# Optimization experiments

Hardware: AMD Instinct MI355X
Metric: run time of the kernel (lower is better)

Reference implementation:

```python
import jax, jax.numpy as jnp
import numpy as np

EXP_CLAMP = 1.0e6
DENOM_EPS = 1e-10
LRELU_ALPHA = 0.01


def setup_inputs() -> dict:
    key = jax.random.key(0)
    k1, k2, k3, k4, k5, k6 = jax.random.split(key, 6)
    B, N, E, F = 4, 16384, 262144, 64
    h = jax.random.normal(k1, (B, N, F), dtype=jnp.float32)
    edge = jax.random.randint(k2, (B, E, 2), 0, N, dtype=jnp.int32)
    edge_num = jax.random.randint(k3, (B,), 1, E, dtype=jnp.int32)
    edge_weight = jax.random.uniform(k4, (B, E), dtype=jnp.float32)
    W = jax.random.normal(k5, (F, F), dtype=jnp.float32) * 0.15  # xavier-ish scale
    a = jax.random.normal(k6, (1, 2 * F), dtype=jnp.float32) * 0.12
    return {"h": h, "edge": edge, "edge_num": edge_num,
            "edge_weight": edge_weight, "W": W, "a": a}


def _seg_sum(src, idx, num_segments):
    # src: [E, ...], idx: [E] -> [num_segments, ...]
    return jax.ops.segment_sum(src, idx, num_segments=num_segments)


def reference(h, edge, edge_num, edge_weight, W, a):
    B, N, Fin = h.shape
    E = edge.shape[1]
    # linear transform: Wh = h @ W^T  -> [B, N, Fout]
    Wh = jnp.einsum('bnf,of->bno', h, W)
    ctr = edge[:, :, 0]  # [B, E]
    nbr = edge[:, :, 1]  # [B, E]
    Wh_c = jnp.take_along_axis(Wh, ctr[:, :, None], axis=1)  # [B, E, Fout]
    Wh_n = jnp.take_along_axis(Wh, nbr[:, :, None], axis=1)  # [B, E, Fout]
    a_input = jnp.concatenate([Wh_c, Wh_n], axis=-1) * edge_weight[:, :, None]
    # attention logits: leakyrelu(a_input @ a^T), squeeze to [B, E]
    att1 = jax.nn.leaky_relu(jnp.einsum('bek,k->be', a_input, a[0]), LRELU_ALPHA)
    # per-batch valid-edge mask (edges beyond edge_num zeroed, as in torch loop)
    mask = (jnp.arange(E, dtype=jnp.int32)[None, :] < edge_num[:, None])
    x_exp = jnp.clip(jnp.exp(att1), 0.0, EXP_CLAMP) * mask.astype(att1.dtype)
    # segment softmax denominator over center nodes
    denom = DENOM_EPS + jax.vmap(_seg_sum, in_axes=(0, 0, None))(x_exp, ctr, N)  # [B, N]
    att = x_exp / jnp.take_along_axis(denom, ctr, axis=1)  # [B, E]
    # weighted neighbor aggregation via scatter-add on center index
    att_Wh = Wh_n * att[:, :, None]  # masked edges already have att == 0
    h_prime = jax.vmap(_seg_sum, in_axes=(0, 0, None))(att_Wh, ctr, N)  # [B, N, Fout]
    return jax.nn.relu(h_prime)
```

## Files before the change

kernel.cpp:

```cpp
#include <hip/hip_runtime.h>

#define BB 4
#define NN 16384
#define EE 262144
#define FF 64
#define ROWS (BB * NN)
#define CAP 64

typedef __bf16 bf16x8 __attribute__((ext_vector_type(8)));
typedef float  f32x4  __attribute__((ext_vector_type(4)));

__device__ __forceinline__ unsigned short f32_to_bf16(float f) {
    unsigned int u = __float_as_uint(f);
    u += 0x7FFFu + ((u >> 16) & 1u);
    return (unsigned short)(u >> 16);
}

__global__ __launch_bounds__(256) void scsn_kernel(
    const float* __restrict__ h, const float* __restrict__ W,
    const float* __restrict__ a,
    float* __restrict__ sc, float* __restrict__ sn, int* __restrict__ cnt)
{
    __shared__ float wc[FF], wn[FF];
    const int t = threadIdx.x;

    if (blockIdx.x < 256) cnt[blockIdx.x * 256 + t] = 0;

    if (t < 128) {
        const int f = t & 63;
        const float* av = a + (t >> 6) * FF;
        float s = 0.0f;
        #pragma unroll 8
        for (int o = 0; o < FF; ++o)
            s = fmaf(av[o], W[o * FF + f], s);
        (t < 64 ? wc : wn)[f] = s;
    }
    __syncthreads();

    const int gl   = t & 15;
    const int rloc = t >> 4;
    const float4 wcv = *(const float4*)&wc[gl * 4];
    const float4 wnv = *(const float4*)&wn[gl * 4];

    for (int base = blockIdx.x * 16; base < ROWS; base += gridDim.x * 16) {
        const int row = base + rloc;
        const float4 hv = ((const float4*)h)[(size_t)row * 16 + gl];
        float s1 = hv.x * wcv.x + hv.y * wcv.y + hv.z * wcv.z + hv.w * wcv.w;
        float s2 = hv.x * wnv.x + hv.y * wnv.y + hv.z * wnv.z + hv.w * wnv.w;
        #pragma unroll
        for (int off = 8; off; off >>= 1) {
            s1 += __shfl_xor(s1, off);
            s2 += __shfl_xor(s2, off);
        }
        if (gl == 0) { sc[row] = s1; sn[row] = s2; }
    }
}

__global__ __launch_bounds__(256) void mfma_bin_kernel(
    const float* __restrict__ h, const float* __restrict__ W,
    const int* __restrict__ edge, const int* __restrict__ edge_num,
    const float* __restrict__ ew,
    const float* __restrict__ sc, const float* __restrict__ sn,
    unsigned short* __restrict__ Wh, int* __restrict__ cnt,
    unsigned int* __restrict__ payload)
{
    const int t = threadIdx.x;
    const int lane = t & 63;
    const int m = lane & 15;
    const int q = lane >> 4;

    bf16x8 bfrag[4][2];
    #pragma unroll
    for (int nt = 0; nt < 4; ++nt) {
        const float* wr = W + (nt * 16 + m) * FF;
        #pragma unroll
        for (int kh = 0; kh < 2; ++kh) {
            const float4 v0 = *(const float4*)(wr + kh * 32 + q * 8);
            const float4 v1 = *(const float4*)(wr + kh * 32 + q * 8 + 4);
            bf16x8 b;
            b[0] = (__bf16)v0.x; b[1] = (__bf16)v0.y;
            b[2] = (__bf16)v0.z; b[3] = (__bf16)v0.w;
            b[4] = (__bf16)v1.x; b[5] = (__bf16)v1.y;
            b[6] = (__bf16)v1.z; b[7] = (__bf16)v1.w;
            bfrag[nt][kh] = b;
        }
    }

    {
        const int waveId = (blockIdx.x * 256 + t) >> 6;
        const int R0 = waveId * 16;
        const float* hr = h + (size_t)(R0 + m) * FF;
        bf16x8 af[2];
        #pragma unroll
        for (int kh = 0; kh < 2; ++kh) {
            const float4 v0 = *(const float4*)(hr + kh * 32 + q * 8);
            const float4 v1 = *(const float4*)(hr + kh * 32 + q * 8 + 4);
            bf16x8 aa;
            aa[0] = (__bf16)v0.x; aa[1] = (__bf16)v0.y;
            aa[2] = (__bf16)v0.z; aa[3] = (__bf16)v0.w;
            aa[4] = (__bf16)v1.x; aa[5] = (__bf16)v1.y;
            aa[6] = (__bf16)v1.z; aa[7] = (__bf16)v1.w;
            af[kh] = aa;
        }
        #pragma unroll
        for (int nt = 0; nt < 4; ++nt) {
            f32x4 acc = {0.f, 0.f, 0.f, 0.f};
            acc = __builtin_amdgcn_mfma_f32_16x16x32_bf16(af[0], bfrag[nt][0], acc, 0, 0, 0);
            acc = __builtin_amdgcn_mfma_f32_16x16x32_bf16(af[1], bfrag[nt][1], acc, 0, 0, 0);
            #pragma unroll
            for (int i = 0; i < 4; ++i)
                Wh[(size_t)(R0 + q * 4 + i) * FF + nt * 16 + m] = f32_to_bf16(acc[i]);
        }
    }

    for (int i2 = blockIdx.x * 256 + t; i2 < (BB * EE) / 2;
         i2 += gridDim.x * 256) {
        const int b  = i2 >> 17;
        const int e0 = (2 * i2) & (EE - 1);
        const int en = edge_num[b];
        if (e0 >= en) continue;
        const int4   e4 = ((const int4*)edge)[i2];
        const float2 w2 = ((const float2*)ew)[i2];
        const int row0 = b * NN + e4.x;
        const int row1 = b * NN + e4.z;
        const bool act1 = (e0 + 1 < en);

        const int pos0 = atomicAdd(&cnt[row0], 1);
        const int pos1 = act1 ? atomicAdd(&cnt[row1], 1) : CAP;

        const float* snB = sn + b * NN;
        float att0 = w2.x * (sc[row0] + snB[e4.y]);
        att0 = att0 > 0.0f ? att0 : 0.01f * att0;
        const float xe0 = fminf(__expf(att0), 1000000.0f);
        unsigned int u0 = (__float_as_uint(xe0) + 0x2000u) & 0xFFFFC000u;
        if (pos0 < CAP)
            payload[(size_t)row0 * CAP + pos0] = u0 | (unsigned int)e4.y;

        if (act1) {
            float att1 = w2.y * (sc[row1] + snB[e4.w]);
            att1 = att1 > 0.0f ? att1 : 0.01f * att1;
            const float xe1 = fminf(__expf(att1), 1000000.0f);
            unsigned int u1 = (__float_as_uint(xe1) + 0x2000u) & 0xFFFFC000u;
            if (pos1 < CAP)
                payload[(size_t)row1 * CAP + pos1] = u1 | (unsigned int)e4.w;
        }
    }
}

__global__ __launch_bounds__(256) void gather_kernel(
    const int* __restrict__ cnt, const unsigned int* __restrict__ payload,
    const uint2* __restrict__ Wh2,
    float* __restrict__ out)
{
    const int bi = blockIdx.x;
    const int xcd = bi & 7;
    const int batch = xcd >> 1;
    const int within = ((bi >> 3) << 1) | (xcd & 1);
    const int rg = batch * 4096 + within;

    const int lane = threadIdx.x & 63;
    const int wave = threadIdx.x >> 6;
    const int row = rg * 4 + wave;
    const int grp = lane >> 4;
    const int gl  = lane & 15;
    int deg = cnt[row];
    if (deg > CAP) deg = CAP;
    const unsigned int* pl = payload + (size_t)row * CAP;
    const uint2* WhB = Wh2 + (size_t)batch * NN * 16;

    float a0 = 0.f, a1 = 0.f, a2 = 0.f, a3 = 0.f, dsum = 0.f;
    const unsigned int p = (lane < deg) ? pl[lane] : 0u;
    for (int jj = 0; jj < deg; jj += 16) {
        const unsigned int pv0 = __shfl(p, jj + grp);
        const unsigned int pv1 = __shfl(p, jj + grp + 4);
        const unsigned int pv2 = __shfl(p, jj + grp + 8);
        const unsigned int pv3 = __shfl(p, jj + grp + 12);
        const uint2 w0 = WhB[(size_t)(pv0 & 0x3FFFu) * 16 + gl];
        const uint2 w1 = WhB[(size_t)(pv1 & 0x3FFFu) * 16 + gl];
        const uint2 w2 = WhB[(size_t)(pv2 & 0x3FFFu) * 16 + gl];
        const uint2 w3 = WhB[(size_t)(pv3 & 0x3FFFu) * 16 + gl];
        const float xe0 = __uint_as_float(pv0 & 0xFFFFC000u);
        const float xe1 = __uint_as_float(pv1 & 0xFFFFC000u);
        const float xe2 = __uint_as_float(pv2 & 0xFFFFC000u);
        const float xe3 = __uint_as_float(pv3 & 0xFFFFC000u);
        a0 = fmaf(xe0, __uint_as_float(w0.x << 16),         a0);
        a1 = fmaf(xe0, __uint_as_float(w0.x & 0xFFFF0000u), a1);
        a2 = fmaf(xe0, __uint_as_float(w0.y << 16),         a2);
        a3 = fmaf(xe0, __uint_as_float(w0.y & 0xFFFF0000u), a3);
        a0 = fmaf(xe1, __uint_as_float(w1.x << 16),         a0);
        a1 = fmaf(xe1, __uint_as_float(w1.x & 0xFFFF0000u), a1);
        a2 = fmaf(xe1, __uint_as_float(w1.y << 16),         a2);
        a3 = fmaf(xe1, __uint_as_float(w1.y & 0xFFFF0000u), a3);
        a0 = fmaf(xe2, __uint_as_float(w2.x << 16),         a0);
        a1 = fmaf(xe2, __uint_as_float(w2.x & 0xFFFF0000u), a1);
        a2 = fmaf(xe2, __uint_as_float(w2.y << 16),         a2);
        a3 = fmaf(xe2, __uint_as_float(w2.y & 0xFFFF0000u), a3);
        a0 = fmaf(xe3, __uint_as_float(w3.x << 16),         a0);
        a1 = fmaf(xe3, __uint_as_float(w3.x & 0xFFFF0000u), a1);
        a2 = fmaf(xe3, __uint_as_float(w3.y << 16),         a2);
        a3 = fmaf(xe3, __uint_as_float(w3.y & 0xFFFF0000u), a3);
        dsum += (xe0 + xe1) + (xe2 + xe3);
    }
    a0 += __shfl_xor(a0, 16); a1 += __shfl_xor(a1, 16);
    a2 += __shfl_xor(a2, 16); a3 += __shfl_xor(a3, 16);
    dsum += __shfl_xor(dsum, 16);
    a0 += __shfl_xor(a0, 32); a1 += __shfl_xor(a1, 32);
    a2 += __shfl_xor(a2, 32); a3 += __shfl_xor(a3, 32);
    dsum += __shfl_xor(dsum, 32);

    if (grp == 0) {
        const float inv = 1.0f / (1e-10f + dsum);
        float4 o;
        o.x = fmaxf(a0 * inv, 0.0f);
        o.y = fmaxf(a1 * inv, 0.0f);
        o.z = fmaxf(a2 * inv, 0.0f);
        o.w = fmaxf(a3 * inv, 0.0f);
        ((float4*)out)[(size_t)row * 16 + gl] = o;
    }
}

extern "C" void kernel_launch(void* const* d_in, const int* in_sizes, int n_in,
                              void* d_out, int out_size, void* d_ws, size_t ws_size,
                              hipStream_t stream)
{
    const float* h        = (const float*)d_in[0];
    const int*   edge     = (const int*)  d_in[1];
    const int*   edge_num = (const int*)  d_in[2];
    const float* ew       = (const float*)d_in[3];
    const float* W        = (const float*)d_in[4];
    const float* a        = (const float*)d_in[5];
    float* out = (float*)d_out;

    unsigned short* Wh = (unsigned short*)d_ws;
    float* sc        = (float*)(Wh + (size_t)BB * NN * FF);
    float* sn        = sc + ROWS;
    int*   cnt       = (int*)(sn + ROWS);
    unsigned int* payload = (unsigned int*)(cnt + ROWS);

    scsn_kernel<<<1024, 256, 0, stream>>>(h, W, a, sc, sn, cnt);

    mfma_bin_kernel<<<1024, 256, 0, stream>>>(h, W, edge, edge_num, ew,
                                              sc, sn, Wh, cnt, payload);

    gather_kernel<<<ROWS / 4, 256, 0, stream>>>(cnt, payload,
                                                (const uint2*)Wh, out);
}
```

Measured before the change: 138.6 us.

## Fold attention scores into MFMA epilogue and defer logit computation to gather

Removes the separate scsn kernel. sc/sn are now computed from the MFMA accumulators by dotting with a and reducing with shuffles. The binning pass stores edge index plus neighbour instead of the precomputed exp weight, and the gather kernel recomputes the attention exp per lane using sc, sn and edge_weight. cnt is zeroed with a memset, and the bin kernel runs with 2048 blocks and one edge pair per thread. This trades a kernel launch and a full pass over h for extra random loads of ew and sn in the gather, and for an Wh-based (bf16-rounded) logit path.

Measured after the change: 148.1 us. 1.07x slower.

```diff
diff --git a/kernel.cpp b/kernel.cpp
--- a/kernel.cpp
+++ b/kernel.cpp
@@ -16,52 +16,12 @@
     return (unsigned short)(u >> 16);
 }
 
-__global__ __launch_bounds__(256) void scsn_kernel(
+__global__ __launch_bounds__(256) void mfma_bin_kernel(
     const float* __restrict__ h, const float* __restrict__ W,
     const float* __restrict__ a,
-    float* __restrict__ sc, float* __restrict__ sn, int* __restrict__ cnt)
-{
-    __shared__ float wc[FF], wn[FF];
-    const int t = threadIdx.x;
-
-    if (blockIdx.x < 256) cnt[blockIdx.x * 256 + t] = 0;
-
-    if (t < 128) {
-        const int f = t & 63;
-        const float* av = a + (t >> 6) * FF;
-        float s = 0.0f;
-        #pragma unroll 8
-        for (int o = 0; o < FF; ++o)
-            s = fmaf(av[o], W[o * FF + f], s);
-        (t < 64 ? wc : wn)[f] = s;
-    }
-    __syncthreads();
-
-    const int gl   = t & 15;
-    const int rloc = t >> 4;
-    const float4 wcv = *(const float4*)&wc[gl * 4];
-    const float4 wnv = *(const float4*)&wn[gl * 4];
-
-    for (int base = blockIdx.x * 16; base < ROWS; base += gridDim.x * 16) {
-        const int row = base + rloc;
-        const float4 hv = ((const float4*)h)[(size_t)row * 16 + gl];
-        float s1 = hv.x * wcv.x + hv.y * wcv.y + hv.z * wcv.z + hv.w * wcv.w;
-        float s2 = hv.x * wnv.x + hv.y * wnv.y + hv.z * wnv.z + hv.w * wnv.w;
-        #pragma unroll
-        for (int off = 8; off; off >>= 1) {
-            s1 += __shfl_xor(s1, off);
-            s2 += __shfl_xor(s2, off);
-        }
-        if (gl == 0) { sc[row] = s1; sn[row] = s2; }
-    }
-}
-
-__global__ __launch_bounds__(256) void mfma_bin_kernel(
-    const float* __restrict__ h, const float* __restrict__ W,
     const int* __restrict__ edge, const int* __restrict__ edge_num,
-    const float* __restrict__ ew,
-    const float* __restrict__ sc, const float* __restrict__ sn,
-    unsigned short* __restrict__ Wh, int* __restrict__ cnt,
+    unsigned short* __restrict__ Wh, float* __restrict__ sc,
+    float* __restrict__ sn, int* __restrict__ cnt,
     unsigned int* __restrict__ payload)
 {
     const int t = threadIdx.x;
@@ -69,25 +29,8 @@
     const int m = lane & 15;
     const int q = lane >> 4;
 
-    bf16x8 bfrag[4][2];
-    #pragma unroll
-    for (int nt = 0; nt < 4; ++nt) {
-        const float* wr = W + (nt * 16 + m) * FF;
-        #pragma unroll
-        for (int kh = 0; kh < 2; ++kh) {
-            const float4 v0 = *(const float4*)(wr + kh * 32 + q * 8);
-            const float4 v1 = *(const float4*)(wr + kh * 32 + q * 8 + 4);
-            bf16x8 b;
-            b[0] = (__bf16)v0.x; b[1] = (__bf16)v0.y;
-            b[2] = (__bf16)v0.z; b[3] = (__bf16)v0.w;
-            b[4] = (__bf16)v1.x; b[5] = (__bf16)v1.y;
-            b[6] = (__bf16)v1.z; b[7] = (__bf16)v1.w;
-            bfrag[nt][kh] = b;
-        }
-    }
-
-    {
-        const int waveId = (blockIdx.x * 256 + t) >> 6;
+    const int waveId = (blockIdx.x * 256 + t) >> 6;
+    if (waveId < ROWS / 16) {
         const int R0 = waveId * 16;
         const float* hr = h + (size_t)(R0 + m) * FF;
         bf16x8 af[2];
@@ -102,54 +45,79 @@
             aa[6] = (__bf16)v1.z; aa[7] = (__bf16)v1.w;
             af[kh] = aa;
         }
+
+        float scv[4] = {0.f, 0.f, 0.f, 0.f};
+        float snv[4] = {0.f, 0.f, 0.f, 0.f};
         #pragma unroll
         for (int nt = 0; nt < 4; ++nt) {
+            const float* wr = W + (nt * 16 + m) * FF;
+            bf16x8 bf[2];
+            #pragma unroll
+            for (int kh = 0; kh < 2; ++kh) {
+                const float4 v0 = *(const float4*)(wr + kh * 32 + q * 8);
+                const float4 v1 = *(const float4*)(wr + kh * 32 + q * 8 + 4);
+                bf16x8 b;
+                b[0] = (__bf16)v0.x; b[1] = (__bf16)v0.y;
+                b[2] = (__bf16)v0.z; b[3] = (__bf16)v0.w;
+                b[4] = (__bf16)v1.x; b[5] = (__bf16)v1.y;
+                b[6] = (__bf16)v1.z; b[7] = (__bf16)v1.w;
+                bf[kh] = b;
+            }
             f32x4 acc = {0.f, 0.f, 0.f, 0.f};
-            acc = __builtin_amdgcn_mfma_f32_16x16x32_bf16(af[0], bfrag[nt][0], acc, 0, 0, 0);
-            acc = __builtin_amdgcn_mfma_f32_16x16x32_bf16(af[1], bfrag[nt][1], acc, 0, 0, 0);
-            #pragma unroll
-            for (int i = 0; i < 4; ++i)
+            acc = __builtin_amdgcn_mfma_f32_16x16x32_bf16(af[0], bf[0], acc, 0, 0, 0);
+            acc = __builtin_amdgcn_mfma_f32_16x16x32_bf16(af[1], bf[1], acc, 0, 0, 0);
+
+            const float acm = a[nt * 16 + m];
+            const float anm = a[FF + nt * 16 + m];
+            #pragma unroll
+            for (int i = 0; i < 4; ++i) {
                 Wh[(size_t)(R0 + q * 4 + i) * FF + nt * 16 + m] = f32_to_bf16(acc[i]);
-        }
-    }
-
-    for (int i2 = blockIdx.x * 256 + t; i2 < (BB * EE) / 2;
-         i2 += gridDim.x * 256) {
-        const int b  = i2 >> 17;
-        const int e0 = (2 * i2) & (EE - 1);
-        const int en = edge_num[b];
-        if (e0 >= en) continue;
-        const int4   e4 = ((const int4*)edge)[i2];
-        const float2 w2 = ((const float2*)ew)[i2];
+                scv[i] = fmaf(acc[i], acm, scv[i]);
+                snv[i] = fmaf(acc[i], anm, snv[i]);
+            }
+        }
+        #pragma unroll
+        for (int i = 0; i < 4; ++i) {
+            #pragma unroll
+            for (int off = 1; off < 16; off <<= 1) {
+                scv[i] += __shfl_xor(scv[i], off);
+                snv[i] += __shfl_xor(snv[i], off);
+            }
+        }
+        if (m == 0) {
+            #pragma unroll
+            for (int i = 0; i < 4; ++i) {
+                sc[R0 + q * 4 + i] = scv[i];
+                sn[R0 + q * 4 + i] = snv[i];
+            }
+        }
+    }
+
+    const int i2 = blockIdx.x * 256 + t;
+    const int b  = i2 >> 17;
+    const int e0 = (2 * i2) & (EE - 1);
+    const int en = edge_num[b];
+    if (e0 < en) {
+        const int4 e4 = ((const int4*)edge)[i2];
         const int row0 = b * NN + e4.x;
-        const int row1 = b * NN + e4.z;
+        const int pos0 = atomicAdd(&cnt[row0], 1);
         const bool act1 = (e0 + 1 < en);
-
-        const int pos0 = atomicAdd(&cnt[row0], 1);
-        const int pos1 = act1 ? atomicAdd(&cnt[row1], 1) : CAP;
-
-        const float* snB = sn + b * NN;
-        float att0 = w2.x * (sc[row0] + snB[e4.y]);
-        att0 = att0 > 0.0f ? att0 : 0.01f * att0;
-        const float xe0 = fminf(__expf(att0), 1000000.0f);
-        unsigned int u0 = (__float_as_uint(xe0) + 0x2000u) & 0xFFFFC000u;
+        int pos1 = CAP, row1 = 0;
+        if (act1) { row1 = b * NN + e4.z; pos1 = atomicAdd(&cnt[row1], 1); }
         if (pos0 < CAP)
-            payload[(size_t)row0 * CAP + pos0] = u0 | (unsigned int)e4.y;
-
-        if (act1) {
-            float att1 = w2.y * (sc[row1] + snB[e4.w]);
-            att1 = att1 > 0.0f ? att1 : 0.01f * att1;
-            const float xe1 = fminf(__expf(att1), 1000000.0f);
-            unsigned int u1 = (__float_as_uint(xe1) + 0x2000u) & 0xFFFFC000u;
-            if (pos1 < CAP)
-                payload[(size_t)row1 * CAP + pos1] = u1 | (unsigned int)e4.w;
-        }
+            payload[(size_t)row0 * CAP + pos0] =
+                ((unsigned int)e0 << 14) | (unsigned int)e4.y;
+        if (act1 && pos1 < CAP)
+            payload[(size_t)row1 * CAP + pos1] =
+                ((unsigned int)(e0 + 1) << 14) | (unsigned int)e4.w;
     }
 }
 
 __global__ __launch_bounds__(256) void gather_kernel(
     const int* __restrict__ cnt, const unsigned int* __restrict__ payload,
     const uint2* __restrict__ Wh2,
+    const float* __restrict__ sc, const float* __restrict__ sn,
+    const float* __restrict__ ew,
     float* __restrict__ out)
 {
     const int bi = blockIdx.x;
@@ -168,8 +136,21 @@
     const unsigned int* pl = payload + (size_t)row * CAP;
     const uint2* WhB = Wh2 + (size_t)batch * NN * 16;
 
+    const unsigned int praw = (lane < deg) ? pl[lane] : 0u;
+    float xe;
+    {
+        const int eidx = (int)(praw >> 14);
+        const int nbr  = (int)(praw & 0x3FFFu);
+        const float we = ew[(size_t)batch * EE + eidx];
+        float att = we * (sc[row] + sn[batch * NN + nbr]);
+        att = att > 0.0f ? att : 0.01f * att;
+        xe = fminf(__expf(att), 1000000.0f);
+        if (lane >= deg) xe = 0.0f;
+    }
+    const unsigned int p = ((__float_as_uint(xe) + 0x2000u) & 0xFFFFC000u)
+                         | (praw & 0x3FFFu);
+
     float a0 = 0.f, a1 = 0.f, a2 = 0.f, a3 = 0.f, dsum = 0.f;
-    const unsigned int p = (lane < deg) ? pl[lane] : 0u;
     for (int jj = 0; jj < deg; jj += 16) {
         const unsigned int pv0 = __shfl(p, jj + grp);
         const unsigned int pv1 = __shfl(p, jj + grp + 4);
@@ -237,11 +218,11 @@
     int*   cnt       = (int*)(sn + ROWS);
     unsigned int* payload = (unsigned int*)(cnt + ROWS);
 
-    scsn_kernel<<<1024, 256, 0, stream>>>(h, W, a, sc, sn, cnt);
-
-    mfma_bin_kernel<<<1024, 256, 0, stream>>>(h, W, edge, edge_num, ew,
-                                              sc, sn, Wh, cnt, payload);
-
-    gather_kernel<<<ROWS / 4, 256, 0, stream>>>(cnt, payload,
-                                                (const uint2*)Wh, out);
-}
+    hipMemsetAsync(cnt, 0, sizeof(int) * ROWS, stream);
+
+    mfma_bin_kernel<<<2048, 256, 0, stream>>>(h, W, a, edge, edge_num,
+                                              Wh, sc, sn, cnt, payload);
+
+    gather_kernel<<<ROWS / 4, 256, 0, stream>>>(cnt, payload, (const uint2*)Wh,
+                                                sc, sn, ew, out);
+}
```

## Split per-row edge bins into eight per-XCD copies to localize atomics

Applied to the files above, without the earlier changes.

The single counter and payload bin arrays are replaced by eight copies, one per XCD group chosen from the block index, each with a capacity of 32 slots. Binning atomics then hit counters that are mostly touched by one XCD, which is meant to cut cross-XCD contention and coherence traffic. The gather kernel reads the eight counts, builds a prefix sum with shuffles, and fetches each lane's payload from the right sub-bin. This costs eight times the counter zeroing and memory, adds extra gather-side work, and truncates edges differently when one sub-bin exceeds 32 entries.

Result: slower. 143.4 us (+3.5%).

```diff
diff --git a/kernel.cpp b/kernel.cpp
--- a/kernel.cpp
+++ b/kernel.cpp
@@ -5,7 +5,7 @@
 #define EE 262144
 #define FF 64
 #define ROWS (BB * NN)
-#define CAP 64
+#define CAPX 32
 
 typedef __bf16 bf16x8 __attribute__((ext_vector_type(8)));
 typedef float  f32x4  __attribute__((ext_vector_type(4)));
@@ -19,12 +19,13 @@
 __global__ __launch_bounds__(256) void scsn_kernel(
     const float* __restrict__ h, const float* __restrict__ W,
     const float* __restrict__ a,
-    float* __restrict__ sc, float* __restrict__ sn, int* __restrict__ cnt)
+    float* __restrict__ sc, float* __restrict__ sn, int* __restrict__ cntx)
 {
     __shared__ float wc[FF], wn[FF];
     const int t = threadIdx.x;
 
-    if (blockIdx.x < 256) cnt[blockIdx.x * 256 + t] = 0;
+    for (int i = blockIdx.x * 256 + t; i < 8 * ROWS; i += 1024 * 256)
+        cntx[i] = 0;
 
     if (t < 128) {
         const int f = t & 63;
@@ -61,8 +62,8 @@
     const int* __restrict__ edge, const int* __restrict__ edge_num,
     const float* __restrict__ ew,
     const float* __restrict__ sc, const float* __restrict__ sn,
-    unsigned short* __restrict__ Wh, int* __restrict__ cnt,
-    unsigned int* __restrict__ payload)
+    unsigned short* __restrict__ Wh, int* __restrict__ cntx,
+    unsigned int* __restrict__ payx)
 {
     const int t = threadIdx.x;
     const int lane = t & 63;
@@ -112,6 +113,10 @@
                 Wh[(size_t)(R0 + q * 4 + i) * FF + nt * 16 + m] = f32_to_bf16(acc[i]);
         }
     }
+
+    const int xg = blockIdx.x & 7;
+    int* cnt = cntx + xg * ROWS;
+    unsigned int* pay = payx + (size_t)xg * ROWS * CAPX;
 
     for (int i2 = blockIdx.x * 256 + t; i2 < (BB * EE) / 2;
          i2 += gridDim.x * 256) {
@@ -126,29 +131,29 @@
         const bool act1 = (e0 + 1 < en);
 
         const int pos0 = atomicAdd(&cnt[row0], 1);
-        const int pos1 = act1 ? atomicAdd(&cnt[row1], 1) : CAP;
+        const int pos1 = act1 ? atomicAdd(&cnt[row1], 1) : CAPX;
 
         const float* snB = sn + b * NN;
         float att0 = w2.x * (sc[row0] + snB[e4.y]);
         att0 = att0 > 0.0f ? att0 : 0.01f * att0;
         const float xe0 = fminf(__expf(att0), 1000000.0f);
         unsigned int u0 = (__float_as_uint(xe0) + 0x2000u) & 0xFFFFC000u;
-        if (pos0 < CAP)
-            payload[(size_t)row0 * CAP + pos0] = u0 | (unsigned int)e4.y;
+        if (pos0 < CAPX)
+            pay[(size_t)row0 * CAPX + pos0] = u0 | (unsigned int)e4.y;
 
         if (act1) {
             float att1 = w2.y * (sc[row1] + snB[e4.w]);
             att1 = att1 > 0.0f ? att1 : 0.01f * att1;
             const float xe1 = fminf(__expf(att1), 1000000.0f);
             unsigned int u1 = (__float_as_uint(xe1) + 0x2000u) & 0xFFFFC000u;
-            if (pos1 < CAP)
-                payload[(size_t)row1 * CAP + pos1] = u1 | (unsigned int)e4.w;
+            if (pos1 < CAPX)
+                pay[(size_t)row1 * CAPX + pos1] = u1 | (unsigned int)e4.w;
         }
     }
 }
 
 __global__ __launch_bounds__(256) void gather_kernel(
-    const int* __restrict__ cnt, const unsigned int* __restrict__ payload,
+    const int* __restrict__ cntx, const unsigned int* __restrict__ payx,
     const uint2* __restrict__ Wh2,
     float* __restrict__ out)
 {
@@ -163,13 +168,40 @@
     const int row = rg * 4 + wave;
     const int grp = lane >> 4;
     const int gl  = lane & 15;
-    int deg = cnt[row];
-    if (deg > CAP) deg = CAP;
-    const unsigned int* pl = payload + (size_t)row * CAP;
     const uint2* WhB = Wh2 + (size_t)batch * NN * 16;
 
+    int myc = 0;
+    if (lane < 8) myc = cntx[lane * ROWS + row];
+    int pref1, pref2, pref3, pref4, pref5, pref6, pref7, pref8;
+    {
+        const int d0 = min(__shfl(myc, 0), CAPX);
+        const int d1 = min(__shfl(myc, 1), CAPX);
+        const int d2 = min(__shfl(myc, 2), CAPX);
+        const int d3 = min(__shfl(myc, 3), CAPX);
+        const int d4 = min(__shfl(myc, 4), CAPX);
+        const int d5 = min(__shfl(myc, 5), CAPX);
+        const int d6 = min(__shfl(myc, 6), CAPX);
+        const int d7 = min(__shfl(myc, 7), CAPX);
+        pref1 = d0;         pref2 = pref1 + d1; pref3 = pref2 + d2;
+        pref4 = pref3 + d3; pref5 = pref4 + d4; pref6 = pref5 + d5;
+        pref7 = pref6 + d6; pref8 = pref7 + d7;
+    }
+    int deg = min(pref8, 64);
+
+    unsigned int p = 0u;
+    if (lane < deg) {
+        int seg = 0, base = 0;
+        if (lane >= pref1) { seg = 1; base = pref1; }
+        if (lane >= pref2) { seg = 2; base = pref2; }
+        if (lane >= pref3) { seg = 3; base = pref3; }
+        if (lane >= pref4) { seg = 4; base = pref4; }
+        if (lane >= pref5) { seg = 5; base = pref5; }
+        if (lane >= pref6) { seg = 6; base = pref6; }
+        if (lane >= pref7) { seg = 7; base = pref7; }
+        p = payx[(size_t)seg * ROWS * CAPX + (size_t)row * CAPX + (lane - base)];
+    }
+
     float a0 = 0.f, a1 = 0.f, a2 = 0.f, a3 = 0.f, dsum = 0.f;
-    const unsigned int p = (lane < deg) ? pl[lane] : 0u;
     for (int jj = 0; jj < deg; jj += 16) {
         const unsigned int pv0 = __shfl(p, jj + grp);
         const unsigned int pv1 = __shfl(p, jj + grp + 4);
@@ -234,14 +266,14 @@
     unsigned short* Wh = (unsigned short*)d_ws;
     float* sc        = (float*)(Wh + (size_t)BB * NN * FF);
     float* sn        = sc + ROWS;
-    int*   cnt       = (int*)(sn + ROWS);
-    unsigned int* payload = (unsigned int*)(cnt + ROWS);
-
-    scsn_kernel<<<1024, 256, 0, stream>>>(h, W, a, sc, sn, cnt);
+    int*   cntx      = (int*)(sn + ROWS);
+    unsigned int* payx = (unsigned int*)(cntx + 8 * ROWS);
+
+    scsn_kernel<<<1024, 256, 0, stream>>>(h, W, a, sc, sn, cntx);
 
     mfma_bin_kernel<<<1024, 256, 0, stream>>>(h, W, edge, edge_num, ew,
-                                              sc, sn, Wh, cnt, payload);
-
-    gather_kernel<<<ROWS / 4, 256, 0, stream>>>(cnt, payload,
+                                              sc, sn, Wh, cntx, payx);
+
+    gather_kernel<<<ROWS / 4, 256, 0, stream>>>(cntx, payx,
                                                 (const uint2*)Wh, out);
 }
```

## Replace capped per-row atomic binning with two-level counting sort into CSR

Applied to the files above, without the earlier changes.

Replaces the fixed-capacity per-row payload slots, filled with global atomics, by a two-level counting sort. Edges are first histogrammed into 256 coarse buckets per chunk, a scan produces offsets, edges are scattered into the buckets, and a per-bucket LDS sort orders them by row to build CSR start offsets. The gather then walks variable-length row ranges and no longer truncates at 64 neighbours. This removes contended global atomics and the scattered payload writes. In exchange it adds two kernel launches, a serial single-block scan, and extra memory traffic for the bucket arrays.

New measurement: 161.1 us. +16.3%, slower.

```diff
diff --git a/kernel.cpp b/kernel.cpp
--- a/kernel.cpp
+++ b/kernel.cpp
@@ -5,7 +5,9 @@
 #define EE 262144
 #define FF 64
 #define ROWS (BB * NN)
-#define CAP 64
+#define CHUNKS 512
+#define CHUNK_E 2048
+#define BCAP 5120
 
 typedef __bf16 bf16x8 __attribute__((ext_vector_type(8)));
 typedef float  f32x4  __attribute__((ext_vector_type(4)));
@@ -16,15 +18,15 @@
     return (unsigned short)(u >> 16);
 }
 
-__global__ __launch_bounds__(256) void scsn_kernel(
+__global__ __launch_bounds__(256) void scsn_hist_kernel(
     const float* __restrict__ h, const float* __restrict__ W,
     const float* __restrict__ a,
-    float* __restrict__ sc, float* __restrict__ sn, int* __restrict__ cnt)
+    const int* __restrict__ edge, const int* __restrict__ edge_num,
+    float* __restrict__ sc, float* __restrict__ sn, int* __restrict__ histArr)
 {
     __shared__ float wc[FF], wn[FF];
+    __shared__ int lhist[256];
     const int t = threadIdx.x;
-
-    if (blockIdx.x < 256) cnt[blockIdx.x * 256 + t] = 0;
 
     if (t < 128) {
         const int f = t & 63;
@@ -41,7 +43,6 @@
     const int rloc = t >> 4;
     const float4 wcv = *(const float4*)&wc[gl * 4];
     const float4 wnv = *(const float4*)&wn[gl * 4];
-
     for (int base = blockIdx.x * 16; base < ROWS; base += gridDim.x * 16) {
         const int row = base + rloc;
         const float4 hv = ((const float4*)h)[(size_t)row * 16 + gl];
@@ -54,39 +55,53 @@
         }
         if (gl == 0) { sc[row] = s1; sn[row] = s2; }
     }
-}
-
-__global__ __launch_bounds__(256) void mfma_bin_kernel(
+
+    if (blockIdx.x < CHUNKS) {
+        lhist[t] = 0;
+        __syncthreads();
+        const int b  = blockIdx.x >> 7;
+        const int en = edge_num[b];
+        const int geBase = blockIdx.x * CHUNK_E;
+        #pragma unroll
+        for (int k = 0; k < 8; ++k) {
+            const int ge = geBase + t + k * 256;
+            if ((ge & (EE - 1)) < en) {
+                const int ctr = edge[2 * (size_t)ge];
+                atomicAdd(&lhist[(b << 6) | (ctr >> 8)], 1);
+            }
+        }
+        __syncthreads();
+        histArr[blockIdx.x * 256 + t] = lhist[t];
+    }
+}
+
+__global__ __launch_bounds__(256) void mfma_scan_kernel(
     const float* __restrict__ h, const float* __restrict__ W,
-    const int* __restrict__ edge, const int* __restrict__ edge_num,
-    const float* __restrict__ ew,
-    const float* __restrict__ sc, const float* __restrict__ sn,
-    unsigned short* __restrict__ Wh, int* __restrict__ cnt,
-    unsigned int* __restrict__ payload)
+    unsigned short* __restrict__ Wh,
+    int* __restrict__ histArr, int* __restrict__ bucketBase,
+    int* __restrict__ startArr)
 {
     const int t = threadIdx.x;
-    const int lane = t & 63;
-    const int m = lane & 15;
-    const int q = lane >> 4;
-
-    bf16x8 bfrag[4][2];
-    #pragma unroll
-    for (int nt = 0; nt < 4; ++nt) {
-        const float* wr = W + (nt * 16 + m) * FF;
-        #pragma unroll
-        for (int kh = 0; kh < 2; ++kh) {
-            const float4 v0 = *(const float4*)(wr + kh * 32 + q * 8);
-            const float4 v1 = *(const float4*)(wr + kh * 32 + q * 8 + 4);
-            bf16x8 b;
-            b[0] = (__bf16)v0.x; b[1] = (__bf16)v0.y;
-            b[2] = (__bf16)v0.z; b[3] = (__bf16)v0.w;
-            b[4] = (__bf16)v1.x; b[5] = (__bf16)v1.y;
-            b[6] = (__bf16)v1.z; b[7] = (__bf16)v1.w;
-            bfrag[nt][kh] = b;
-        }
-    }
-
-    {
+    if (blockIdx.x < 1024) {
+        const int lane = t & 63;
+        const int m = lane & 15;
+        const int q = lane >> 4;
+        bf16x8 bfrag[4][2];
+        #pragma unroll
+        for (int nt = 0; nt < 4; ++nt) {
+            const float* wr = W + (nt * 16 + m) * FF;
+            #pragma unroll
+            for (int kh = 0; kh < 2; ++kh) {
+                const float4 v0 = *(const float4*)(wr + kh * 32 + q * 8);
+                const float4 v1 = *(const float4*)(wr + kh * 32 + q * 8 + 4);
+                bf16x8 b;
+                b[0] = (__bf16)v0.x; b[1] = (__bf16)v0.y;
+                b[2] = (__bf16)v0.z; b[3] = (__bf16)v0.w;
+                b[4] = (__bf16)v1.x; b[5] = (__bf16)v1.y;
+                b[6] = (__bf16)v1.z; b[7] = (__bf16)v1.w;
+                bfrag[nt][kh] = b;
+            }
+        }
         const int waveId = (blockIdx.x * 256 + t) >> 6;
         const int R0 = waveId * 16;
         const float* hr = h + (size_t)(R0 + m) * FF;
@@ -111,46 +126,110 @@
             for (int i = 0; i < 4; ++i)
                 Wh[(size_t)(R0 + q * 4 + i) * FF + nt * 16 + m] = f32_to_bf16(acc[i]);
         }
-    }
-
-    for (int i2 = blockIdx.x * 256 + t; i2 < (BB * EE) / 2;
-         i2 += gridDim.x * 256) {
-        const int b  = i2 >> 17;
-        const int e0 = (2 * i2) & (EE - 1);
-        const int en = edge_num[b];
-        if (e0 >= en) continue;
-        const int4   e4 = ((const int4*)edge)[i2];
-        const float2 w2 = ((const float2*)ew)[i2];
-        const int row0 = b * NN + e4.x;
-        const int row1 = b * NN + e4.z;
-        const bool act1 = (e0 + 1 < en);
-
-        const int pos0 = atomicAdd(&cnt[row0], 1);
-        const int pos1 = act1 ? atomicAdd(&cnt[row1], 1) : CAP;
-
-        const float* snB = sn + b * NN;
-        float att0 = w2.x * (sc[row0] + snB[e4.y]);
-        att0 = att0 > 0.0f ? att0 : 0.01f * att0;
-        const float xe0 = fminf(__expf(att0), 1000000.0f);
-        unsigned int u0 = (__float_as_uint(xe0) + 0x2000u) & 0xFFFFC000u;
-        if (pos0 < CAP)
-            payload[(size_t)row0 * CAP + pos0] = u0 | (unsigned int)e4.y;
-
-        if (act1) {
-            float att1 = w2.y * (sc[row1] + snB[e4.w]);
-            att1 = att1 > 0.0f ? att1 : 0.01f * att1;
-            const float xe1 = fminf(__expf(att1), 1000000.0f);
-            unsigned int u1 = (__float_as_uint(xe1) + 0x2000u) & 0xFFFFC000u;
-            if (pos1 < CAP)
-                payload[(size_t)row1 * CAP + pos1] = u1 | (unsigned int)e4.w;
-        }
-    }
+    } else {
+        __shared__ int sarr[256];
+        int run = 0;
+        for (int blk = 0; blk < CHUNKS; ++blk) {
+            const int idx = blk * 256 + t;
+            const int v = histArr[idx];
+            histArr[idx] = run;
+            run += v;
+        }
+        sarr[t] = run;
+        __syncthreads();
+        int excl = 0;
+        for (int i = 0; i < 256; ++i) {
+            const int v = sarr[i];
+            if (i < t) excl += v;
+        }
+        bucketBase[t] = excl;
+        if (t == 255) {
+            bucketBase[256] = excl + run;
+            startArr[ROWS] = excl + run;
+        }
+    }
+}
+
+__global__ __launch_bounds__(256) void scatter_kernel(
+    const int* __restrict__ edge, const int* __restrict__ edge_num,
+    const float* __restrict__ ew,
+    const float* __restrict__ sc, const float* __restrict__ sn,
+    const int* __restrict__ histArr, const int* __restrict__ bucketBase,
+    unsigned int* __restrict__ bucketArr, unsigned char* __restrict__ rowlowArr)
+{
+    __shared__ int lbase[256];
+    const int t = threadIdx.x;
+    lbase[t] = histArr[blockIdx.x * 256 + t] + bucketBase[t];
+    __syncthreads();
+
+    const int b  = blockIdx.x >> 7;
+    const int en = edge_num[b];
+    const float* snB = sn + b * NN;
+    const int geBase = blockIdx.x * CHUNK_E;
+    #pragma unroll
+    for (int k = 0; k < 8; ++k) {
+        const int ge = geBase + t + k * 256;
+        if ((ge & (EE - 1)) >= en) continue;
+        const int2 e2 = ((const int2*)edge)[ge];
+        const int row = b * NN + e2.x;
+        float att = ew[ge] * (sc[row] + snB[e2.y]);
+        att = att > 0.0f ? att : 0.01f * att;
+        const float xe = fminf(__expf(att), 1000000.0f);
+        const unsigned int u =
+            ((__float_as_uint(xe) + 0x2000u) & 0xFFFFC000u) | (unsigned int)e2.y;
+        const int bkt = (b << 6) | (e2.x >> 8);
+        const int dst = atomicAdd(&lbase[bkt], 1);
+        bucketArr[dst] = u;
+        rowlowArr[dst] = (unsigned char)(e2.x & 255);
+    }
+}
+
+__global__ __launch_bounds__(256) void bsort_kernel(
+    const unsigned int* __restrict__ bucketArr,
+    const unsigned char* __restrict__ rowlowArr,
+    const int* __restrict__ bucketBase,
+    unsigned int* __restrict__ payloadG, int* __restrict__ startArr)
+{
+    __shared__ unsigned int lpay[BCAP];
+    __shared__ unsigned int lsort[BCAP];
+    __shared__ unsigned char llow[BCAP];
+    __shared__ int lhist[256];
+    __shared__ int rankb[256];
+    const int t = threadIdx.x;
+    const int bkt = blockIdx.x;
+    const int base = bucketBase[bkt];
+    int S = bucketBase[bkt + 1] - base;
+    if (S > BCAP) S = BCAP;
+
+    lhist[t] = 0;
+    __syncthreads();
+    for (int i = t; i < S; i += 256) {
+        lpay[i] = bucketArr[base + i];
+        const unsigned char lo = rowlowArr[base + i];
+        llow[i] = lo;
+        atomicAdd(&lhist[lo], 1);
+    }
+    __syncthreads();
+    int excl = 0;
+    for (int i = 0; i < 256; ++i) {
+        const int v = lhist[i];
+        if (i < t) excl += v;
+    }
+    rankb[t] = excl;
+    startArr[bkt * 256 + t] = base + excl;
+    __syncthreads();
+    for (int i = t; i < S; i += 256) {
+        const int d = atomicAdd(&rankb[llow[i]], 1);
+        lsort[d] = lpay[i];
+    }
+    __syncthreads();
+    for (int i = t; i < S; i += 256)
+        payloadG[base + i] = lsort[i];
 }
 
 __global__ __launch_bounds__(256) void gather_kernel(
-    const int* __restrict__ cnt, const unsigned int* __restrict__ payload,
-    const uint2* __restrict__ Wh2,
-    float* __restrict__ out)
+    const int* __restrict__ startArr, const unsigned int* __restrict__ payloadG,
+    const uint2* __restrict__ Wh2, float* __restrict__ out)
 {
     const int bi = blockIdx.x;
     const int xcd = bi & 7;
@@ -163,43 +242,46 @@
     const int row = rg * 4 + wave;
     const int grp = lane >> 4;
     const int gl  = lane & 15;
-    int deg = cnt[row];
-    if (deg > CAP) deg = CAP;
-    const unsigned int* pl = payload + (size_t)row * CAP;
+    const int s = startArr[row];
+    const int e = startArr[row + 1];
     const uint2* WhB = Wh2 + (size_t)batch * NN * 16;
 
     float a0 = 0.f, a1 = 0.f, a2 = 0.f, a3 = 0.f, dsum = 0.f;
-    const unsigned int p = (lane < deg) ? pl[lane] : 0u;
-    for (int jj = 0; jj < deg; jj += 16) {
-        const unsigned int pv0 = __shfl(p, jj + grp);
-        const unsigned int pv1 = __shfl(p, jj + grp + 4);
-        const unsigned int pv2 = __shfl(p, jj + grp + 8);
-        const unsigned int pv3 = __shfl(p, jj + grp + 12);
-        const uint2 w0 = WhB[(size_t)(pv0 & 0x3FFFu) * 16 + gl];
-        const uint2 w1 = WhB[(size_t)(pv1 & 0x3FFFu) * 16 + gl];
-        const uint2 w2 = WhB[(size_t)(pv2 & 0x3FFFu) * 16 + gl];
-        const uint2 w3 = WhB[(size_t)(pv3 & 0x3FFFu) * 16 + gl];
-        const float xe0 = __uint_as_float(pv0 & 0xFFFFC000u);
-        const float xe1 = __uint_as_float(pv1 & 0xFFFFC000u);
-        const float xe2 = __uint_as_float(pv2 & 0xFFFFC000u);
-        const float xe3 = __uint_as_float(pv3 & 0xFFFFC000u);
-        a0 = fmaf(xe0, __uint_as_float(w0.x << 16),         a0);
-        a1 = fmaf(xe0, __uint_as_float(w0.x & 0xFFFF0000u), a1);
-        a2 = fmaf(xe0, __uint_as_float(w0.y << 16),         a2);
-        a3 = fmaf(xe0, __uint_as_float(w0.y & 0xFFFF0000u), a3);
-        a0 = fmaf(xe1, __uint_as_float(w1.x << 16),         a0);
-        a1 = fmaf(xe1, __uint_as_float(w1.x & 0xFFFF0000u), a1);
-        a2 = fmaf(xe1, __uint_as_float(w1.y << 16),         a2);
-        a3 = fmaf(xe1, __uint_as_float(w1.y & 0xFFFF0000u), a3);
-        a0 = fmaf(xe2, __uint_as_float(w2.x << 16),         a0);
-        a1 = fmaf(xe2, __uint_as_float(w2.x & 0xFFFF0000u), a1);
-        a2 = fmaf(xe2, __uint_as_float(w2.y << 16),         a2);
-        a3 = fmaf(xe2, __uint_as_float(w2.y & 0xFFFF0000u), a3);
-        a0 = fmaf(xe3, __uint_as_float(w3.x << 16),         a0);
-        a1 = fmaf(xe3, __uint_as_float(w3.x & 0xFFFF0000u), a1);
-        a2 = fmaf(xe3, __uint_as_float(w3.y << 16),         a2);
-        a3 = fmaf(xe3, __uint_as_float(w3.y & 0xFFFF0000u), a3);
-        dsum += (xe0 + xe1) + (xe2 + xe3);
+    for (int chunk = s; chunk < e; chunk += 64) {
+        const int j = chunk + lane;
+        const unsigned int p = (j < e) ? payloadG[j] : 0u;
+        const int cend = min(64, e - chunk);
+        for (int jj = 0; jj < cend; jj += 16) {
+            const unsigned int pv0 = __shfl(p, jj + grp);
+            const unsigned int pv1 = __shfl(p, jj + grp + 4);
+            const unsigned int pv2 = __shfl(p, jj + grp + 8);
+            const unsigned int pv3 = __shfl(p, jj + grp + 12);
+            const uint2 w0 = WhB[(size_t)(pv0 & 0x3FFFu) * 16 + gl];
+            const uint2 w1 = WhB[(size_t)(pv1 & 0x3FFFu) * 16 + gl];
+            const uint2 w2 = WhB[(size_t)(pv2 & 0x3FFFu) * 16 + gl];
+            const uint2 w3 = WhB[(size_t)(pv3 & 0x3FFFu) * 16 + gl];
+            const float xe0 = __uint_as_float(pv0 & 0xFFFFC000u);
+            const float xe1 = __uint_as_float(pv1 & 0xFFFFC000u);
+            const float xe2 = __uint_as_float(pv2 & 0xFFFFC000u);
+            const float xe3 = __uint_as_float(pv3 & 0xFFFFC000u);
+            a0 = fmaf(xe0, __uint_as_float(w0.x << 16),         a0);
+            a1 = fmaf(xe0, __uint_as_float(w0.x & 0xFFFF0000u), a1);
+            a2 = fmaf(xe0, __uint_as_float(w0.y << 16),         a2);
+            a3 = fmaf(xe0, __uint_as_float(w0.y & 0xFFFF0000u), a3);
+            a0 = fmaf(xe1, __uint_as_float(w1.x << 16),         a0);
+            a1 = fmaf(xe1, __uint_as_float(w1.x & 0xFFFF0000u), a1);
+            a2 = fmaf(xe1, __uint_as_float(w1.y << 16),         a2);
+            a3 = fmaf(xe1, __uint_as_float(w1.y & 0xFFFF0000u), a3);
+            a0 = fmaf(xe2, __uint_as_float(w2.x << 16),         a0);
+            a1 = fmaf(xe2, __uint_as_float(w2.x & 0xFFFF0000u), a1);
+            a2 = fmaf(xe2, __uint_as_float(w2.y << 16),         a2);
+            a3 = fmaf(xe2, __uint_as_float(w2.y & 0xFFFF0000u), a3);
+            a0 = fmaf(xe3, __uint_as_float(w3.x << 16),         a0);
+            a1 = fmaf(xe3, __uint_as_float(w3.x & 0xFFFF0000u), a1);
+            a2 = fmaf(xe3, __uint_as_float(w3.y << 16),         a2);
+            a3 = fmaf(xe3, __uint_as_float(w3.y & 0xFFFF0000u), a3);
+            dsum += (xe0 + xe1) + (xe2 + xe3);
+        }
     }
     a0 += __shfl_xor(a0, 16); a1 += __shfl_xor(a1, 16);
     a2 += __shfl_xor(a2, 16); a3 += __shfl_xor(a3, 16);
@@ -234,14 +316,26 @@
     unsigned short* Wh = (unsigned short*)d_ws;
     float* sc        = (float*)(Wh + (size_t)BB * NN * FF);
     float* sn        = sc + ROWS;
-    int*   cnt       = (int*)(sn + ROWS);
-    unsigned int* payload = (unsigned int*)(cnt + ROWS);
-
-    scsn_kernel<<<1024, 256, 0, stream>>>(h, W, a, sc, sn, cnt);
-
-    mfma_bin_kernel<<<1024, 256, 0, stream>>>(h, W, edge, edge_num, ew,
-                                              sc, sn, Wh, cnt, payload);
-
-    gather_kernel<<<ROWS / 4, 256, 0, stream>>>(cnt, payload,
+    int*   histArr   = (int*)(sn + ROWS);
+    int*   bucketBase= histArr + CHUNKS * 256;
+    int*   startArr  = bucketBase + 260;
+    unsigned int* bucketArr = (unsigned int*)(startArr + ROWS + 4);
+    unsigned char* rowlowArr = (unsigned char*)(bucketArr + BB * EE);
+    unsigned int* payloadG = (unsigned int*)(rowlowArr + BB * EE);
+
+    scsn_hist_kernel<<<1024, 256, 0, stream>>>(h, W, a, edge, edge_num,
+                                               sc, sn, histArr);
+
+    mfma_scan_kernel<<<1025, 256, 0, stream>>>(h, W, Wh, histArr, bucketBase,
+                                               startArr);
+
+    scatter_kernel<<<CHUNKS, 256, 0, stream>>>(edge, edge_num, ew, sc, sn,
+                                               histArr, bucketBase,
+                                               bucketArr, rowlowArr);
+
+    bsort_kernel<<<256, 256, 0, stream>>>(bucketArr, rowlowArr, bucketBase,
+                                          payloadG, startArr);
+
+    gather_kernel<<<ROWS / 4, 256, 0, stream>>>(startArr, payloadG,
                                                 (const uint2*)Wh, out);
 }
```
